# Kernel optimization log

Measured on AMD Instinct MI355X. Metric: run time of the kernel, lower is better.

The kernel has to match this reference:

```python
import jax, jax.numpy as jnp
import numpy as np

# dims
N_USER = 30000; N_ITEM = 30000; HID = 256; HEADS = 4; DH = HID // HEADS
L = 2; E_BUYS = 200000
IMG_D = 512; TASTE_D = 768; NUTR_D = 20; LR = 64; IMG_RANK = 64
EPS = 1e-5
# node type order: 0=user 1=item 2=taste 3=intention 4=image
# edge type order: taste->item, intention->item, image->item, user->item (buys), item->user (bought_by)


def _bn(x, g, b):
    # nn.BatchNorm1d in training mode (biased variance), deterministic
    mu = jnp.mean(x, axis=0)
    var = jnp.mean((x - mu) ** 2, axis=0)
    return (x - mu) * jax.lax.rsqrt(var + EPS) * g + b


def _segment_softmax(logits, seg, n):
    m = jax.ops.segment_max(logits, seg, num_segments=n)
    m = jnp.where(jnp.isfinite(m), m, 0.0)
    e = jnp.exp(logits - m[seg])
    s = jax.ops.segment_sum(e, seg, num_segments=n)
    return e / (s[seg] + 1e-16)


def _model(p, user_id, item_id, buys_src, buys_dst):
    # --- encoders (dropout = identity in eval) ---
    xu = jax.nn.relu(_bn(p['user_emb'][user_id] @ p['user_W'] + p['user_b'], p['user_bn_g'], p['user_bn_b']))
    xi = jax.nn.relu(_bn(p['item_emb'][item_id] @ p['item_W'] + p['item_b'], p['item_bn_g'], p['item_bn_b']))
    ximg = (p['image_feat'] @ p['img_U']) @ p['img_V'] + p['img_b']  # LowRankLinear
    xt = p['taste_feat'] @ p['taste_W'] + p['taste_b']
    xn = p['intent_feat'] @ p['intent_W'] + p['intent_b']
    xs = [xu, xi, xt, xn, ximg]
    assoc = jnp.arange(N_ITEM, dtype=jnp.int32)
    # (src_type, dst_type, src_idx, dst_idx)
    edges = [(2, 1, assoc, assoc), (3, 1, assoc, assoc), (4, 1, assoc, assoc),
             (0, 1, buys_src, buys_dst), (1, 0, buys_dst, buys_src)]
    scale = 1.0 / np.sqrt(DH)
    n_of = [N_USER, N_ITEM]
    for l in range(L):
        k, q, v = [], [], []
        for t in range(5):
            kqv = xs[t] @ p['kqv_W'][l, t] + p['kqv_b'][l, t]
            kk, qq, vv = jnp.split(kqv, 3, axis=1)
            k.append(kk.reshape(-1, HEADS, DH))
            q.append(qq.reshape(-1, HEADS, DH))
            v.append(vv.reshape(-1, HEADS, DH))
        buf = {0: [], 1: []}
        for e, (s, d, si, di) in enumerate(edges):
            # relation-specific per-head transforms of source k/v (all src nodes, then gather)
            ke = jnp.einsum('nhd,hde->nhe', k[s], p['k_rel'][l, e])
            ve = jnp.einsum('nhd,hde->nhe', v[s], p['v_rel'][l, e])
            logit = jnp.sum(q[d][di] * ke[si], axis=-1) * p['p_rel'][l, e] * scale  # [E,H]
            buf[d].append((logit, ve[si], di))
        new_xs = list(xs)
        for d in (0, 1):  # dst node types: user, item
            logits = jnp.concatenate([b[0] for b in buf[d]], axis=0)
            msgs = jnp.concatenate([b[1] for b in buf[d]], axis=0)
            dsts = jnp.concatenate([b[2] for b in buf[d]], axis=0)
            alpha = _segment_softmax(logits, dsts, n_of[d])  # softmax over ALL incoming edges per dst node
            agg = jax.ops.segment_sum(alpha[:, :, None] * msgs, dsts, num_segments=n_of[d])
            o = jax.nn.gelu(agg.reshape(-1, HID), approximate=False) @ p['out_W'][l, d] + p['out_b'][l, d]
            sg = jax.nn.sigmoid(p['skip'][l, d])
            o = sg * o + (1.0 - sg) * xs[d]  # HGTConv learned skip
            o = o + xs[d]                    # MultiModalFusionGAT residual
            o = jax.nn.relu(_bn(o, p['fbn_g'][l, d], p['fbn_b'][l, d]))  # per-type BN+ReLU (dropout eval)
            new_xs[d] = o
        xs = new_xs  # taste/intention/image pass through unchanged
    return jnp.stack(xs, axis=0)  # [5, 30000, HID]


def setup_inputs():
    key = jax.random.key(0)
    ks = iter(jax.random.split(key, 48))
    def nrm(shape, scale=0.05):
        return jax.random.normal(next(ks), shape, dtype=jnp.float32) * scale
    z = lambda *s: jnp.zeros(s, jnp.float32)
    o = lambda *s: jnp.ones(s, jnp.float32)
    inp = {}
    inp['user_id'] = jnp.arange(N_USER, dtype=jnp.int32)
    inp['item_id'] = jnp.arange(N_ITEM, dtype=jnp.int32)
    inp['buys_src'] = jax.random.randint(next(ks), (E_BUYS,), 0, N_USER, dtype=jnp.int32)
    inp['buys_dst'] = jax.random.randint(next(ks), (E_BUYS,), 0, N_ITEM, dtype=jnp.int32)
    inp['image_feat'] = nrm((N_ITEM, IMG_D), 1.0)
    inp['taste_feat'] = nrm((N_ITEM, TASTE_D), 1.0)
    inp['intent_feat'] = nrm((N_ITEM, NUTR_D), 1.0)
    inp['user_emb'] = nrm((N_USER, LR), 0.1)
    inp['user_W'] = nrm((LR, HID)); inp['user_b'] = z(HID)
    inp['user_bn_g'] = o(HID); inp['user_bn_b'] = z(HID)
    inp['item_emb'] = nrm((N_ITEM, LR), 0.1)
    inp['item_W'] = nrm((LR, HID)); inp['item_b'] = z(HID)
    inp['item_bn_g'] = o(HID); inp['item_bn_b'] = z(HID)
    inp['img_U'] = nrm((IMG_D, IMG_RANK)); inp['img_V'] = nrm((IMG_RANK, HID)); inp['img_b'] = z(HID)
    inp['taste_W'] = nrm((TASTE_D, HID)); inp['taste_b'] = z(HID)
    inp['intent_W'] = nrm((NUTR_D, HID)); inp['intent_b'] = z(HID)
    inp['kqv_W'] = nrm((L, 5, HID, 3 * HID)); inp['kqv_b'] = z(L, 5, 3 * HID)
    inp['out_W'] = nrm((L, 5, HID, HID)); inp['out_b'] = z(L, 5, HID)
    inp['k_rel'] = nrm((L, 5, HEADS, DH, DH))
    inp['v_rel'] = nrm((L, 5, HEADS, DH, DH))
    inp['p_rel'] = o(L, 5, HEADS)
    inp['skip'] = o(L, 5)
    inp['fbn_g'] = o(L, 2, HID); inp['fbn_b'] = z(L, 2, HID)
    return inp


def reference(user_id, item_id, buys_src, buys_dst, image_feat, taste_feat, intent_feat,
              user_emb, user_W, user_b, user_bn_g, user_bn_b,
              item_emb, item_W, item_b, item_bn_g, item_bn_b,
              img_U, img_V, img_b, taste_W, taste_b, intent_W, intent_b,
              kqv_W, kqv_b, out_W, out_b, k_rel, v_rel, p_rel, skip, fbn_g, fbn_b):
    p = dict(image_feat=image_feat, taste_feat=taste_feat, intent_feat=intent_feat,
             user_emb=user_emb, user_W=user_W, user_b=user_b, user_bn_g=user_bn_g, user_bn_b=user_bn_b,
             item_emb=item_emb, item_W=item_W, item_b=item_b, item_bn_g=item_bn_g, item_bn_b=item_bn_b,
             img_U=img_U, img_V=img_V, img_b=img_b, taste_W=taste_W, taste_b=taste_b,
             intent_W=intent_W, intent_b=intent_b, kqv_W=kqv_W, kqv_b=kqv_b, out_W=out_W, out_b=out_b,
             k_rel=k_rel, v_rel=v_rel, p_rel=p_rel, skip=skip, fbn_g=fbn_g, fbn_b=fbn_b)
    return _model(p, user_id, item_id, buys_src, buys_dst)
```

## Files before the change

### kernel.cpp

```cpp
#include <hip/hip_runtime.h>
#include <math.h>

#define HID 256
#define EBUY 200000
#define NNODE 30000
#define MP 30080
static const size_t S  = (size_t)NNODE * HID;
static const size_t SP = (size_t)MP * HID;

typedef __attribute__((ext_vector_type(8))) short  short8;
typedef __attribute__((ext_vector_type(4))) float  f32x4;

#define OFF_TASTE 0
#define OFF_INT   196608
#define OFF_IMGU  204800
#define OFF_IMGV  237568
#define OFF_USER  253952
#define OFF_ITEM  270336
#define OFF_OUTW  286720
#define WENC_TOT  548864

__device__ __forceinline__ float gelu_f(float x) {
    return 0.5f * x * (1.0f + erff(x * 0.70710678118654752f));
}
__device__ __forceinline__ unsigned short f2bf(float f) {
    unsigned u = __float_as_uint(f);
    u = (u + 0x7FFFu + ((u >> 16) & 1u)) >> 16;
    return (unsigned short)u;
}
__device__ __forceinline__ float b2f(unsigned short us) {
    return __uint_as_float((unsigned)us << 16);
}
__device__ __forceinline__ void gl_lds16(const unsigned short* g, unsigned short* l) {
    __builtin_amdgcn_global_load_lds(
        (const __attribute__((address_space(1))) unsigned int*)g,
        (__attribute__((address_space(3))) unsigned int*)l, 16, 0, 0);
}

__global__ void conv_pad(const float* __restrict__ in, unsigned short* __restrict__ o,
                         int M, int K, int Kpad)
{
    int i = blockIdx.x * 256 + threadIdx.x;
    if (i >= M * Kpad) return;
    int r = i / Kpad, k = i % Kpad;
    o[i] = (k < K) ? f2bf(in[(size_t)r * K + k]) : (unsigned short)0;
}

__global__ void wtconv_all(const float* __restrict__ taste_W, const float* __restrict__ intent_W,
                           const float* __restrict__ img_U, const float* __restrict__ img_V,
                           const float* __restrict__ user_W, const float* __restrict__ item_W,
                           const float* __restrict__ out_W, unsigned short* __restrict__ WENC)
{
    int i = blockIdx.x * 256 + threadIdx.x;
    if (i >= WENC_TOT) return;
    const float* W; int K, N, Kpad, idx;
    if (i < OFF_INT)        { W = taste_W;  K = 768; N = 256; Kpad = 768; idx = i - OFF_TASTE; }
    else if (i < OFF_IMGU)  { W = intent_W; K = 20;  N = 256; Kpad = 32;  idx = i - OFF_INT; }
    else if (i < OFF_IMGV)  { W = img_U;    K = 512; N = 64;  Kpad = 512; idx = i - OFF_IMGU; }
    else if (i < OFF_USER)  { W = img_V;    K = 64;  N = 256; Kpad = 64;  idx = i - OFF_IMGV; }
    else if (i < OFF_ITEM)  { W = user_W;   K = 64;  N = 256; Kpad = 64;  idx = i - OFF_USER; }
    else if (i < OFF_OUTW)  { W = item_W;   K = 64;  N = 256; Kpad = 64;  idx = i - OFF_ITEM; }
    else {
        int k = (i - OFF_OUTW) >> 16;
        int l = k >> 1, d = k & 1;
        W = out_W + (size_t)(l * 5 + d) * 65536;
        K = 256; N = 256; Kpad = 256; idx = (i - OFF_OUTW) & 65535;
    }
    int n = idx / Kpad, kk = idx % Kpad;
    WENC[i] = (kk < K) ? f2bf(W[(size_t)kk * N + n]) : (unsigned short)0;
}

__global__ void build_kqv(const float* __restrict__ kqv_W, const float* __restrict__ kqv_b,
                          const float* __restrict__ k_rel, const float* __restrict__ v_rel,
                          unsigned short* __restrict__ WKV, float* __restrict__ bKV,
                          unsigned short* __restrict__ WQ, float* __restrict__ bQ)
{
    int s = blockIdx.y;
    int l = s / 5, t = s % 5;
    static const int es[5] = {3, 4, 0, 1, 2};
    int e = es[t];
    int tid = blockIdx.x * 256 + threadIdx.x;
    if (tid >= 257 * 768) return;
    int r = tid / 768, c = tid % 768;
    int cb = c >> 8, cc = c & 255;
    int h = cc >> 6, dd = cc & 63;
    const float* W = kqv_W + (size_t)s * 196608;
    const float* bv = kqv_b + (size_t)s * 768;
    const float* Wrow = (r < 256) ? (W + (size_t)r * 768) : bv;
    if (cb == 1) {
        if (t >= 2) return;
        float outv = Wrow[256 + cc];
        if (r < 256) WQ[(size_t)(l * 2 + t) * 65536 + (size_t)cc * 256 + r] = f2bf(outv);
        else         bQ[(l * 2 + t) * 256 + cc] = outv;
        return;
    }
    const float* R = ((cb == 0) ? k_rel : v_rel) + (size_t)(l * 5 + e) * 16384 + (size_t)h * 4096;
    int sb = (cb == 0) ? 0 : 512;
    float sum = 0.f;
    #pragma unroll 8
    for (int d = 0; d < 64; ++d)
        sum += Wrow[sb + h * 64 + d] * R[d * 64 + dd];
    int col = (cb == 0) ? cc : 256 + cc;
    if (r < 256) WKV[(size_t)s * 131072 + (size_t)col * 256 + r] = f2bf(sum);
    else         bKV[s * 512 + col] = sum;
}

template<int AF32, int GATH2, int BSEL, int EPI>
__launch_bounds__(256)
__global__ void gemm_mfma(const void* __restrict__ Ap, const void* __restrict__ Ap2,
                          const int* __restrict__ g1, const int* __restrict__ g2,
                          const unsigned short* __restrict__ BT0, int bStride,
                          const float* __restrict__ bias0, const float* __restrict__ bias1,
                          int biasStride,
                          float* __restrict__ D0, unsigned short* __restrict__ Db,
                          unsigned short* __restrict__ Db2,
                          int M, int N, int K,
                          const float* __restrict__ skipP, const float* __restrict__ resid,
                          float* __restrict__ bns)
{
    __shared__ union {
        unsigned short AB[4][4096];
        unsigned short O[16384];
    } sm;
    const int tid = threadIdx.x;
    const int gx = gridDim.x;
    int bid = blockIdx.y * gx + blockIdx.x;
    {
        int nwg = gx * gridDim.y;
        int q = nwg >> 3, r = nwg & 7;
        int xc = bid & 7, i = bid >> 3;
        int base = (xc < r) ? xc * (q + 1) : r * (q + 1) + (xc - r) * q;
        bid = base + i;
    }
    const int bx = bid % gx, by = bid / gx;
    const int row0 = by * 128, col0 = bx * 128;
    const int wid = tid >> 6, lane = tid & 63;
    const int wr = wid >> 1, wc = wid & 1;
    const int l16 = lane & 15, kg = lane >> 4;
    const int tt = (BSEL || GATH2) ? (by / 235) : 0;

    const unsigned short* BT = BT0 + (size_t)tt * bStride;
    const float* bias = bias0;
    if (GATH2)              bias = tt ? bias1 : bias0;
    else if (BSEL && bias0) bias = bias0 + (size_t)tt * biasStride;

    f32x4 acc[4][4];
    const f32x4 zero = {0.f, 0.f, 0.f, 0.f};
    #pragma unroll
    for (int i = 0; i < 4; ++i)
        #pragma unroll
        for (int j = 0; j < 4; ++j) acc[i][j] = zero;

    const int lrow = lane >> 2, lchk = lane & 3;
    int cB0 = min(col0 + wid * 32 + lrow, N - 1);
    int cB1 = min(col0 + wid * 32 + 16 + lrow, N - 1);
    const unsigned short* Bp0 = BT + (size_t)cB0 * K + lchk * 8;
    const unsigned short* Bp1 = BT + (size_t)cB1 * K + lchk * 8;
    const int ofs0 = wid * 1024;
    const int ofs1 = wid * 1024 + 512;

    const unsigned short* Ap0b = nullptr; const unsigned short* Ap1b = nullptr;
    const float* Af0 = nullptr; const float* Af1 = nullptr;
    const int rA0 = tid >> 2, rA1 = (tid >> 2) + 64;
    const int q0 = tid & 3;
    if (GATH2) {
        int lr0 = row0 + rA0 - tt * MP; if (lr0 >= NNODE) lr0 = NNODE - 1;
        int lr1 = row0 + rA1 - tt * MP; if (lr1 >= NNODE) lr1 = NNODE - 1;
        const int* gA = tt ? g2 : g1;
        const float* Abase = tt ? (const float*)Ap2 : (const float*)Ap;
        Af0 = Abase + (size_t)gA[lr0] * K;
        Af1 = Abase + (size_t)gA[lr1] * K;
    } else if (AF32) {
        Af0 = (const float*)Ap + (size_t)min(row0 + rA0, M - 1) * K;
        Af1 = (const float*)Ap + (size_t)min(row0 + rA1, M - 1) * K;
    } else {
        int rr0 = min(row0 + wid * 32 + lrow, M - 1);
        int rr1 = min(row0 + wid * 32 + 16 + lrow, M - 1);
        Ap0b = (const unsigned short*)Ap + (size_t)rr0 * K + lchk * 8;
        Ap1b = (const unsigned short*)Ap + (size_t)rr1 * K + lchk * 8;
    }

    const int nt = K >> 5;
    int cur = 0;
    #define STAGE(c, k0) do { \
        if (AF32 || GATH2) { \
            float4 x0 = *(const float4*)&Af0[(k0) + q0 * 8]; \
            float4 x1 = *(const float4*)&Af0[(k0) + q0 * 8 + 4]; \
            float4 y0 = *(const float4*)&Af1[(k0) + q0 * 8]; \
            float4 y1 = *(const float4*)&Af1[(k0) + q0 * 8 + 4]; \
            ushort4 u0 = {f2bf(x0.x), f2bf(x0.y), f2bf(x0.z), f2bf(x0.w)}; \
            ushort4 u1 = {f2bf(x1.x), f2bf(x1.y), f2bf(x1.z), f2bf(x1.w)}; \
            ushort4 w0 = {f2bf(y0.x), f2bf(y0.y), f2bf(y0.z), f2bf(y0.w)}; \
            ushort4 w1 = {f2bf(y1.x), f2bf(y1.y), f2bf(y1.z), f2bf(y1.w)}; \
            *(ushort4*)&sm.AB[c][rA0 * 32 + q0 * 8]     = u0; \
            *(ushort4*)&sm.AB[c][rA0 * 32 + q0 * 8 + 4] = u1; \
            *(ushort4*)&sm.AB[c][rA1 * 32 + q0 * 8]     = w0; \
            *(ushort4*)&sm.AB[c][rA1 * 32 + q0 * 8 + 4] = w1; \
        } else { \
            gl_lds16(Ap0b + (k0), &sm.AB[c][ofs0]); \
            gl_lds16(Ap1b + (k0), &sm.AB[c][ofs1]); \
        } \
        gl_lds16(Bp0 + (k0), &sm.AB[2 + (c)][ofs0]); \
        gl_lds16(Bp1 + (k0), &sm.AB[2 + (c)][ofs1]); \
    } while (0)

    STAGE(0, 0);
    __syncthreads();
    for (int s = 0; s < nt; ++s) {
        if (s + 1 < nt) STAGE(cur ^ 1, (s + 1) * 32);
        short8 af[4], bfr[4];
        #pragma unroll
        for (int i = 0; i < 4; ++i) {
            af[i]  = *(const short8*)&sm.AB[cur][(wr * 64 + i * 16 + l16) * 32 + kg * 8];
            bfr[i] = *(const short8*)&sm.AB[2 + cur][(wc * 64 + i * 16 + l16) * 32 + kg * 8];
        }
        #pragma unroll
        for (int i = 0; i < 4; ++i)
            #pragma unroll
            for (int j = 0; j < 4; ++j)
                acc[i][j] = __builtin_amdgcn_mfma_f32_16x16x32_bf16(af[i], bfr[j], acc[i][j], 0, 0, 0);
        __syncthreads();
        cur ^= 1;
    }
    #undef STAGE

    float sg = 0.f;
    if (EPI == 2) sg = 1.f / (1.f + __expf(-skipP[0]));
    #pragma unroll
    for (int j = 0; j < 4; ++j) {
        int lc = wc * 64 + j * 16 + l16;
        int cc = col0 + lc;
        float cs = 0.f, cs2 = 0.f;
        float bv = (bias && cc < N) ? bias[cc] : 0.f;
        #pragma unroll
        for (int i = 0; i < 4; ++i) {
            #pragma unroll
            for (int r = 0; r < 4; ++r) {
                int lr = wr * 64 + i * 16 + kg * 4 + r;
                int rr = row0 + lr;
                float v = acc[i][j][r] + bv;
                if (EPI == 0) {
                    if (D0 && cc < N && rr < M) D0[(size_t)rr * N + cc] = v;
                    sm.O[lr * 128 + ((((lc >> 3) ^ (lr & 7)) << 3) | (lc & 7))] = f2bf(v);
                } else if (EPI == 4 || EPI == 5) {
                    sm.O[lr * 128 + ((((lc >> 3) ^ (lr & 7)) << 3) | (lc & 7))] = f2bf(v);
                } else if (EPI == 6) {
                    D0[(size_t)rr * 256 + cc] = v;
                } else if (EPI == 2) {
                    if (rr < M) {
                        float xo = resid[(size_t)rr * 256 + cc];
                        float o = sg * v + (2.f - sg) * xo;
                        D0[(size_t)rr * 256 + cc] = o;
                        cs += o; cs2 += o * o;
                    }
                }
            }
        }
        if (EPI == 2) {
            cs  += __shfl_xor(cs, 16);  cs  += __shfl_xor(cs, 32);
            cs2 += __shfl_xor(cs2, 16); cs2 += __shfl_xor(cs2, 32);
            if (kg == 0 && cc < N) {
                atomicAdd(&bns[cc], cs);
                atomicAdd(&bns[256 + cc], cs2);
            }
        }
    }
    if (EPI == 0 || EPI == 4 || EPI == 5) {
        __syncthreads();
        unsigned short* T; int ldN, cofs;
        if (EPI == 4)      { T = (col0 < 256) ? Db : Db2; ldN = 256; cofs = col0 & 255; }
        else if (EPI == 5) { T = Db; ldN = 256; cofs = col0; }
        else               { T = Db; ldN = N;   cofs = col0; }
        int nloc = N - col0; if (nloc > 128) nloc = 128;
        if (nloc >= 128) {
            int lr = tid >> 1, half = tid & 1;
            int rr = row0 + lr;
            if (EPI != 0 || rr < M) {
                uint4* dst = (uint4*)&T[(size_t)rr * ldN + cofs + half * 64];
                #pragma unroll
                for (int c = 0; c < 8; ++c) {
                    int ch = half * 8 + c;
                    dst[c] = *(const uint4*)&sm.O[lr * 128 + ((ch ^ (lr & 7)) << 3)];
                }
            }
        } else {
            if (tid < 128) {
                int lr = tid, rr = row0 + lr;
                if (rr < M) {
                    uint4* dst = (uint4*)&T[(size_t)rr * ldN + cofs];
                    #pragma unroll
                    for (int c = 0; c < 8; ++c)
                        dst[c] = *(const uint4*)&sm.O[lr * 128 + ((c ^ (lr & 7)) << 3)];
                }
            }
        }
    }
}

__global__ void edge_hist2(const int* __restrict__ dstk, const int* __restrict__ srck,
                           int* __restrict__ cnt)
{
    int j = blockIdx.x * 256 + threadIdx.x;
    if (j < EBUY) atomicAdd(&cnt[dstk[j]], 1);
    else if (j < 2 * EBUY) atomicAdd(&cnt[NNODE + srck[j - EBUY]], 1);
}

#define SCAN_NB 30
#define SCAN_CH 1000
__global__ void scan_part(const int* __restrict__ cnt, int* __restrict__ bt)
{
    int set = blockIdx.y;
    const int* c = cnt + set * NNODE;
    int b = blockIdx.x;
    int i = b * SCAN_CH + threadIdx.x;
    int v = (threadIdx.x < SCAN_CH && i < NNODE) ? c[i] : 0;
    __shared__ int wsum[16];
    int lane = threadIdx.x & 63, wv = threadIdx.x >> 6;
    for (int o = 32; o; o >>= 1) v += __shfl_down(v, o);
    if (lane == 0) wsum[wv] = v;
    __syncthreads();
    if (threadIdx.x == 0) {
        int s = 0;
        for (int w = 0; w < 16; ++w) s += wsum[w];
        bt[set * 32 + b] = s;
    }
}

__global__ void scan_mid(int* __restrict__ bt, int* __restrict__ off_i, int* __restrict__ off_u)
{
    int set = threadIdx.x;
    if (set >= 2) return;
    int* b = bt + set * 32;
    int s = 0;
    for (int i = 0; i < SCAN_NB; ++i) { int c = b[i]; b[i] = s; s += c; }
    (set ? off_u : off_i)[NNODE] = s;
}

__global__ void scan_final(const int* __restrict__ cnt, const int* __restrict__ bt,
                           int* __restrict__ off_i, int* __restrict__ off_u,
                           int* __restrict__ cur_i, int* __restrict__ cur_u)
{
    int set = blockIdx.y;
    const int* c = cnt + set * NNODE;
    int* off = set ? off_u : off_i;
    int* cur = set ? cur_u : cur_i;
    int b = blockIdx.x;
    int i = b * SCAN_CH + threadIdx.x;
    int v = (threadIdx.x < SCAN_CH && i < NNODE) ? c[i] : 0;
    int lane = threadIdx.x & 63, wv = threadIdx.x >> 6;
    int x = v;
    for (int o = 1; o < 64; o <<= 1) { int t = __shfl_up(x, o); if (lane >= o) x += t; }
    __shared__ int wtot[16];
    if (lane == 63) wtot[wv] = x;
    __syncthreads();
    if (wv == 0) {
        int y = (lane < 16) ? wtot[lane] : 0;
        for (int o = 1; o < 16; o <<= 1) { int t = __shfl_up(y, o); if (lane >= o) y += t; }
        if (lane < 16) wtot[lane] = y;
    }
    __syncthreads();
    int wbase = (wv == 0) ? 0 : wtot[wv - 1];
    int excl = bt[set * 32 + b] + wbase + x - v;
    if (threadIdx.x < SCAN_CH && i < NNODE) { off[i] = excl; cur[i] = excl; }
}

__global__ void edge_place2(const int* __restrict__ dstk, const int* __restrict__ srck,
                            int* __restrict__ cur_i, int* __restrict__ cur_u,
                            int* __restrict__ src_i, int* __restrict__ src_u)
{
    int j = blockIdx.x * 256 + threadIdx.x;
    if (j < EBUY) {
        int pos = atomicAdd(&cur_i[dstk[j]], 1);
        src_i[pos] = srck[j];
    } else if (j < 2 * EBUY) {
        int j2 = j - EBUY;
        int pos = atomicAdd(&cur_u[srck[j2]], 1);
        src_u[pos] = dstk[j2];
    }
}

template<int HAS_ASSOC>
__launch_bounds__(256)
__global__ void attn_gather(const unsigned short* __restrict__ Qd,
                            const unsigned short* __restrict__ KEs,
                            const unsigned short* __restrict__ VEs,
                            const unsigned short* __restrict__ KEa,
                            const unsigned short* __restrict__ VEa,
                            const int* __restrict__ roff, const int* __restrict__ srcArr,
                            const float* __restrict__ pR,
                            unsigned short* __restrict__ AGGb)
{
    int wid = (blockIdx.x * 256 + threadIdx.x) >> 6;
    int lane = threadIdx.x & 63;
    if (wid >= NNODE) return;
    int h = lane >> 4;

    ushort4 qb = *(const ushort4*)(Qd + (size_t)wid * 256 + lane * 4);
    float4 q = {b2f(qb.x), b2f(qb.y), b2f(qb.z), b2f(qb.w)};
    float m = -INFINITY, s = 0.f;
    float4 acc = {0.f, 0.f, 0.f, 0.f};

    if (HAS_ASSOC) {
        #pragma unroll
        for (int e = 0; e < 3; ++e) {
            ushort4 kb = *(const ushort4*)(KEa + (size_t)e * SP + (size_t)wid * 256 + lane * 4);
            float d = q.x * b2f(kb.x) + q.y * b2f(kb.y) + q.z * b2f(kb.z) + q.w * b2f(kb.w);
            for (int off = 8; off; off >>= 1) d += __shfl_xor(d, off, 16);
            float lg = d * pR[e * 4 + h] * 0.125f;
            ushort4 vv = *(const ushort4*)(VEa + (size_t)e * SP + (size_t)wid * 256 + lane * 4);
            float mn = fmaxf(m, lg);
            float so = __expf(m - mn);
            float ev = __expf(lg - mn);
            s = s * so + ev;
            acc.x = acc.x * so + ev * b2f(vv.x);
            acc.y = acc.y * so + ev * b2f(vv.y);
            acc.z = acc.z * so + ev * b2f(vv.z);
            acc.w = acc.w * so + ev * b2f(vv.w);
            m = mn;
        }
    }

    float pb = pR[(HAS_ASSOC ? 12 : 16) + h] * 0.125f;
    int j1 = roff[wid + 1];
    for (int j = roff[wid]; j < j1; ++j) {
        int src = srcArr[j];
        ushort4 kb = *(const ushort4*)(KEs + (size_t)src * 256 + lane * 4);
        float d = q.x * b2f(kb.x) + q.y * b2f(kb.y) + q.z * b2f(kb.z) + q.w * b2f(kb.w);
        for (int off = 8; off; off >>= 1) d += __shfl_xor(d, off, 16);
        float lg = d * pb;
        ushort4 vv = *(const ushort4*)(VEs + (size_t)src * 256 + lane * 4);
        float mn = fmaxf(m, lg);
        float so = __expf(m - mn);
        float ev = __expf(lg - mn);
        s = s * so + ev;
        acc.x = acc.x * so + ev * b2f(vv.x);
        acc.y = acc.y * so + ev * b2f(vv.y);
        acc.z = acc.z * so + ev * b2f(vv.z);
        acc.w = acc.w * so + ev * b2f(vv.w);
        m = mn;
    }

    float inv = 1.f / (s + 1e-16f);
    ushort4 o4;
    o4.x = f2bf(gelu_f(acc.x * inv));
    o4.y = f2bf(gelu_f(acc.y * inv));
    o4.z = f2bf(gelu_f(acc.z * inv));
    o4.w = f2bf(gelu_f(acc.w * inv));
    *(ushort4*)(AGGb + (size_t)wid * 256 + lane * 4) = o4;
}

#define BNB 512
__global__ void bn_stats2(const float* __restrict__ SCRf, float* __restrict__ part)
{
    int tt = blockIdx.y;
    const float* x = SCRf + (size_t)tt * SP;
    int col = threadIdx.x;
    int b = blockIdx.x;
    float s = 0.f, s2 = 0.f;
    int r = b;
    for (; r + 3 * BNB < NNODE; r += 4 * BNB) {
        float v0 = x[(size_t)r * 256 + col];
        float v1 = x[(size_t)(r + BNB) * 256 + col];
        float v2 = x[(size_t)(r + 2 * BNB) * 256 + col];
        float v3 = x[(size_t)(r + 3 * BNB) * 256 + col];
        s += v0 + v1 + v2 + v3;
        s2 += v0 * v0 + v1 * v1 + v2 * v2 + v3 * v3;
    }
    for (; r < NNODE; r += BNB) {
        float v = x[(size_t)r * 256 + col];
        s += v; s2 += v * v;
    }
    part[((size_t)tt * BNB + b) * 512 + col] = s;
    part[((size_t)tt * BNB + b) * 512 + 256 + col] = s2;
}

__global__ void bn_fin2(const float* __restrict__ part,
                        const float* __restrict__ g0, const float* __restrict__ b0,
                        const float* __restrict__ g1, const float* __restrict__ b1,
                        float* __restrict__ scsh)
{
    int tid = threadIdx.x;
    int tt = tid >> 8, col = tid & 255;
    const float* p = part + (size_t)tt * BNB * 512;
    float s = 0.f, s2 = 0.f;
    #pragma unroll 4
    for (int b = 0; b < BNB; ++b) { s += p[b * 512 + col]; s2 += p[b * 512 + 256 + col]; }
    float mu = s / (float)NNODE;
    float var = s2 / (float)NNODE - mu * mu;
    float sc = rsqrtf(var + 1e-5f) * (tt ? g1 : g0)[col];
    scsh[tt * 512 + col] = sc;
    scsh[tt * 512 + 256 + col] = (tt ? b1 : b0)[col] - mu * sc;
}

__global__ void bn_apply2(const float* __restrict__ SCRf, const float* __restrict__ scsh,
                          float* __restrict__ out, unsigned short* __restrict__ XBall)
{
    const int Q4 = NNODE * 64;
    for (int i = blockIdx.x * 256 + threadIdx.x; i < 2 * Q4; i += gridDim.x * 256) {
        int tt = (i >= Q4) ? 1 : 0;
        int local = i - tt * Q4;
        int c4 = local & 63;
        float4 sc4 = *(const float4*)&scsh[tt * 512 + c4 * 4];
        float4 sh4 = *(const float4*)&scsh[tt * 512 + 256 + c4 * 4];
        float4 v = ((const float4*)(SCRf + (size_t)tt * SP))[local];
        v.x = fmaxf(v.x * sc4.x + sh4.x, 0.f);
        v.y = fmaxf(v.y * sc4.y + sh4.y, 0.f);
        v.z = fmaxf(v.z * sc4.z + sh4.z, 0.f);
        v.w = fmaxf(v.w * sc4.w + sh4.w, 0.f);
        ((float4*)(out + (size_t)tt * S))[local] = v;
        ushort4 u = {f2bf(v.x), f2bf(v.y), f2bf(v.z), f2bf(v.w)};
        ((ushort4*)(XBall + (size_t)tt * SP))[local] = u;
    }
}

__global__ void bn_find(const float* __restrict__ bns, const float* __restrict__ g,
                        const float* __restrict__ b_, float* __restrict__ scsh)
{
    int col = threadIdx.x;
    float s = bns[col], s2 = bns[256 + col];
    float mu = s / (float)NNODE;
    float var = s2 / (float)NNODE - mu * mu;
    float sc = rsqrtf(var + 1e-5f) * g[col];
    scsh[col] = sc;
    scsh[256 + col] = b_[col] - mu * sc;
}

__global__ void bn_apply1(const float* __restrict__ x, const float* __restrict__ scsh,
                          float* __restrict__ y, unsigned short* __restrict__ yb)
{
    const int Q4 = NNODE * 64;
    int c4 = threadIdx.x & 63;
    float4 sc4 = *(const float4*)&scsh[c4 * 4];
    float4 sh4 = *(const float4*)&scsh[256 + c4 * 4];
    for (int i = blockIdx.x * 256 + threadIdx.x; i < Q4; i += gridDim.x * 256) {
        float4 v = ((const float4*)x)[i];
        v.x = fmaxf(v.x * sc4.x + sh4.x, 0.f);
        v.y = fmaxf(v.y * sc4.y + sh4.y, 0.f);
        v.z = fmaxf(v.z * sc4.z + sh4.z, 0.f);
        v.w = fmaxf(v.w * sc4.w + sh4.w, 0.f);
        ((float4*)y)[i] = v;
        ushort4 u = {f2bf(v.x), f2bf(v.y), f2bf(v.z), f2bf(v.w)};
        ((ushort4*)yb)[i] = u;
    }
}

extern "C" void kernel_launch(void* const* d_in, const int* in_sizes, int n_in,
                              void* d_out, int out_size, void* d_ws, size_t ws_size,
                              hipStream_t stream)
{
    const int*   user_id    = (const int*)d_in[0];
    const int*   item_id    = (const int*)d_in[1];
    const int*   buys_src   = (const int*)d_in[2];
    const int*   buys_dst   = (const int*)d_in[3];
    const float* image_feat = (const float*)d_in[4];
    const float* taste_feat = (const float*)d_in[5];
    const float* intent_feat= (const float*)d_in[6];
    const float* user_emb   = (const float*)d_in[7];
    const float* user_W     = (const float*)d_in[8];
    const float* user_b     = (const float*)d_in[9];
    const float* user_bn_g  = (const float*)d_in[10];
    const float* user_bn_b  = (const float*)d_in[11];
    const float* item_emb   = (const float*)d_in[12];
    const float* item_W     = (const float*)d_in[13];
    const float* item_b     = (const float*)d_in[14];
    const float* item_bn_g  = (const float*)d_in[15];
    const float* item_bn_b  = (const float*)d_in[16];
    const float* img_U      = (const float*)d_in[17];
    const float* img_V      = (const float*)d_in[18];
    const float* img_b      = (const float*)d_in[19];
    const float* taste_W    = (const float*)d_in[20];
    const float* taste_b    = (const float*)d_in[21];
    const float* intent_W   = (const float*)d_in[22];
    const float* intent_b   = (const float*)d_in[23];
    const float* kqv_W      = (const float*)d_in[24];
    const float* kqv_b      = (const float*)d_in[25];
    const float* out_W      = (const float*)d_in[26];
    const float* out_b      = (const float*)d_in[27];
    const float* k_rel      = (const float*)d_in[28];
    const float* v_rel      = (const float*)d_in[29];
    const float* p_rel      = (const float*)d_in[30];
    const float* skip       = (const float*)d_in[31];
    const float* fbn_g      = (const float*)d_in[32];
    const float* fbn_b      = (const float*)d_in[33];

    float* out = (float*)d_out;
    float* ws  = (float*)d_ws;

    float* SCRf = ws;
    float* BNSp = SCRf + 2 * SP;
    float* BNS  = BNSp + 2 * BNB * 512;
    float* SCSH = BNS + 512;
    float* bKV  = SCSH + 1024;
    float* bQ   = bKV + 5120;
    unsigned short* QB    = (unsigned short*)(bQ + 1024);
    unsigned short* XBall = QB + 2 * SP;
    unsigned short* KEall = XBall + 5 * SP;
    unsigned short* VEall = KEall + 5 * SP;
    unsigned short* AGB   = VEall + 5 * SP;
    unsigned short* IMB   = AGB + S;
    unsigned short* IPB   = IMB + (size_t)NNODE * 64;
    unsigned short* WKV   = IPB + (size_t)NNODE * 32;
    unsigned short* WQ    = WKV + 1310720;
    unsigned short* WENC  = WQ + 262144;
    int* cnt   = (int*)(WENC + WENC_TOT);
    int* off_i = cnt + 2 * NNODE;
    int* off_u = off_i + NNODE + 1;
    int* cur_i = off_u + NNODE + 1;
    int* cur_u = cur_i + NNODE;
    int* src_i = cur_u + NNODE;
    int* src_u = src_i + EBUY;
    int* bt    = src_u + EBUY;

    size_t need = (size_t)((char*)(bt + 64) - (char*)ws);
    if (ws_size < need) return;

    hipMemsetAsync(cnt, 0, 2 * NNODE * 4, stream);
    edge_hist2<<<(2 * EBUY + 255) / 256, 256, 0, stream>>>(buys_dst, buys_src, cnt);
    scan_part<<<dim3(SCAN_NB, 2), 1024, 0, stream>>>(cnt, bt);
    scan_mid<<<1, 64, 0, stream>>>(bt, off_i, off_u);
    scan_final<<<dim3(SCAN_NB, 2), 1024, 0, stream>>>(cnt, bt, off_i, off_u, cur_i, cur_u);
    edge_place2<<<(2 * EBUY + 255) / 256, 256, 0, stream>>>(buys_dst, buys_src, cur_i, cur_u, src_i, src_u);

    wtconv_all<<<(WENC_TOT + 255) / 256, 256, 0, stream>>>(taste_W, intent_W, img_U, img_V,
                                                           user_W, item_W, out_W, WENC);
    build_kqv<<<dim3(771, 10), 256, 0, stream>>>(kqv_W, kqv_b, k_rel, v_rel, WKV, bKV, WQ, bQ);
    conv_pad<<<(NNODE * 32 + 255) / 256, 256, 0, stream>>>(intent_feat, IPB, NNODE, 20, 32);

    hipLaunchKernelGGL((gemm_mfma<1,0,0,0>), dim3(2,235), dim3(256), 0, stream,
        taste_feat, nullptr, nullptr, nullptr, WENC + OFF_TASTE, 0, taste_b, nullptr, 0,
        out + 2*S, XBall + 2*SP, nullptr, NNODE, 256, 768, nullptr, nullptr, nullptr);
    hipLaunchKernelGGL((gemm_mfma<0,0,0,0>), dim3(2,235), dim3(256), 0, stream,
        IPB, nullptr, nullptr, nullptr, WENC + OFF_INT, 0, intent_b, nullptr, 0,
        out + 3*S, XBall + 3*SP, nullptr, NNODE, 256, 32, nullptr, nullptr, nullptr);
    hipLaunchKernelGGL((gemm_mfma<1,0,0,0>), dim3(1,235), dim3(256), 0, stream,
        image_feat, nullptr, nullptr, nullptr, WENC + OFF_IMGU, 0, nullptr, nullptr, 0,
        nullptr, IMB, nullptr, NNODE, 64, 512, nullptr, nullptr, nullptr);
    hipLaunchKernelGGL((gemm_mfma<0,0,0,0>), dim3(2,235), dim3(256), 0, stream,
        IMB, nullptr, nullptr, nullptr, WENC + OFF_IMGV, 0, img_b, nullptr, 0,
        out + 4*S, XBall + 4*SP, nullptr, NNODE, 256, 64, nullptr, nullptr, nullptr);
    hipLaunchKernelGGL((gemm_mfma<1,1,1,6>), dim3(2,470), dim3(256), 0, stream,
        user_emb, item_emb, user_id, item_id, WENC + OFF_USER, 16384, user_b, item_b, 0,
        SCRf, nullptr, nullptr, 2*MP, 256, 64, nullptr, nullptr, nullptr);
    bn_stats2<<<dim3(BNB, 2), 256, 0, stream>>>(SCRf, BNSp);
    bn_fin2<<<1, 512, 0, stream>>>(BNSp, user_bn_g, user_bn_b, item_bn_g, item_bn_b, SCSH);
    bn_apply2<<<960, 256, 0, stream>>>(SCRf, SCSH, out, XBall);

    for (int l = 0; l < 2; ++l) {
        hipLaunchKernelGGL((gemm_mfma<0,0,1,4>), dim3(4, 5*235), dim3(256), 0, stream,
            XBall, nullptr, nullptr, nullptr, WKV + (size_t)l*5*131072, 131072,
            bKV + l*5*512, nullptr, 512, nullptr, KEall, VEall,
            5*MP, 512, 256, nullptr, nullptr, nullptr);
        hipLaunchKernelGGL((gemm_mfma<0,0,1,5>), dim3(2, 2*235), dim3(256), 0, stream,
            XBall, nullptr, nullptr, nullptr, WQ + (size_t)l*2*65536, 65536,
            bQ + l*2*256, nullptr, 256, nullptr, QB, nullptr,
            2*MP, 256, 256, nullptr, nullptr, nullptr);
        hipLaunchKernelGGL((attn_gather<1>), dim3((NNODE*64 + 255)/256), dim3(256), 0, stream,
            QB + SP, KEall, VEall, KEall + 2*SP, VEall + 2*SP, off_i, src_i,
            p_rel + l*20, AGB);
        hipMemsetAsync(BNS, 0, 512 * 4, stream);
        hipLaunchKernelGGL((gemm_mfma<0,0,0,2>), dim3(2,235), dim3(256), 0, stream,
            AGB, nullptr, nullptr, nullptr, WENC + OFF_OUTW + (size_t)(l*2+1)*65536, 0,
            out_b + (l*5+1)*256, nullptr, 0, SCRf, nullptr, nullptr,
            NNODE, 256, 256, skip + (l*5+1), out + S, BNS);
        bn_find<<<1, 256, 0, stream>>>(BNS, fbn_g + (l*2+1)*256, fbn_b + (l*2+1)*256, SCSH);
        bn_apply1<<<960, 256, 0, stream>>>(SCRf, SCSH, out + S, XBall + SP);
        hipLaunchKernelGGL((attn_gather<0>), dim3((NNODE*64 + 255)/256), dim3(256), 0, stream,
            QB, KEall + SP, VEall + SP, nullptr, nullptr, off_u, src_u,
            p_rel + l*20, AGB);
        hipMemsetAsync(BNS, 0, 512 * 4, stream);
        hipLaunchKernelGGL((gemm_mfma<0,0,0,2>), dim3(2,235), dim3(256), 0, stream,
            AGB, nullptr, nullptr, nullptr, WENC + OFF_OUTW + (size_t)(l*2+0)*65536, 0,
            out_b + (l*5+0)*256, nullptr, 0, SCRf, nullptr, nullptr,
            NNODE, 256, 256, skip + (l*5+0), out, BNS);
        bn_find<<<1, 256, 0, stream>>>(BNS, fbn_g + (l*2+0)*256, fbn_b + (l*2+0)*256, SCSH);
        bn_apply1<<<960, 256, 0, stream>>>(SCRf, SCSH, out, XBall);
    }
}
```

Measured before the change: 1.085 ms.

## Pipeline bf16 GEMM with explicit vmcnt waits and prefetch edge gathers

Splits the GEMM main loop into an fp32-convert path and a bf16 direct-to-LDS path. The bf16 path replaces __syncthreads with explicit s_waitcnt vmcnt plus raw s_barrier, so the next tile's global-to-LDS loads stay in flight while the current tile is computed, and it raises wave priority around the MFMA block. In the attention aggregation, the next edge's K/V rows are loaded one iteration ahead to hide gather latency. The hand-written waitcnt values depend on exactly four outstanding loads per stage, which is fragile if the compiler inserts other memory operations.

```diff
diff --git a/kernel.cpp b/kernel.cpp
--- a/kernel.cpp
+++ b/kernel.cpp
@@ -182,47 +182,83 @@
 
     const int nt = K >> 5;
     int cur = 0;
-    #define STAGE(c, k0) do { \
-        if (AF32 || GATH2) { \
-            float4 x0 = *(const float4*)&Af0[(k0) + q0 * 8]; \
-            float4 x1 = *(const float4*)&Af0[(k0) + q0 * 8 + 4]; \
-            float4 y0 = *(const float4*)&Af1[(k0) + q0 * 8]; \
-            float4 y1 = *(const float4*)&Af1[(k0) + q0 * 8 + 4]; \
-            ushort4 u0 = {f2bf(x0.x), f2bf(x0.y), f2bf(x0.z), f2bf(x0.w)}; \
-            ushort4 u1 = {f2bf(x1.x), f2bf(x1.y), f2bf(x1.z), f2bf(x1.w)}; \
-            ushort4 w0 = {f2bf(y0.x), f2bf(y0.y), f2bf(y0.z), f2bf(y0.w)}; \
-            ushort4 w1 = {f2bf(y1.x), f2bf(y1.y), f2bf(y1.z), f2bf(y1.w)}; \
-            *(ushort4*)&sm.AB[c][rA0 * 32 + q0 * 8]     = u0; \
-            *(ushort4*)&sm.AB[c][rA0 * 32 + q0 * 8 + 4] = u1; \
-            *(ushort4*)&sm.AB[c][rA1 * 32 + q0 * 8]     = w0; \
-            *(ushort4*)&sm.AB[c][rA1 * 32 + q0 * 8 + 4] = w1; \
-        } else { \
-            gl_lds16(Ap0b + (k0), &sm.AB[c][ofs0]); \
-            gl_lds16(Ap1b + (k0), &sm.AB[c][ofs1]); \
-        } \
+
+    #define STAGE_F32(c, k0) do { \
+        float4 x0 = *(const float4*)&Af0[(k0) + q0 * 8]; \
+        float4 x1 = *(const float4*)&Af0[(k0) + q0 * 8 + 4]; \
+        float4 y0 = *(const float4*)&Af1[(k0) + q0 * 8]; \
+        float4 y1 = *(const float4*)&Af1[(k0) + q0 * 8 + 4]; \
+        ushort4 u0 = {f2bf(x0.x), f2bf(x0.y), f2bf(x0.z), f2bf(x0.w)}; \
+        ushort4 u1 = {f2bf(x1.x), f2bf(x1.y), f2bf(x1.z), f2bf(x1.w)}; \
+        ushort4 w0 = {f2bf(y0.x), f2bf(y0.y), f2bf(y0.z), f2bf(y0.w)}; \
+        ushort4 w1 = {f2bf(y1.x), f2bf(y1.y), f2bf(y1.z), f2bf(y1.w)}; \
+        *(ushort4*)&sm.AB[c][rA0 * 32 + q0 * 8]     = u0; \
+        *(ushort4*)&sm.AB[c][rA0 * 32 + q0 * 8 + 4] = u1; \
+        *(ushort4*)&sm.AB[c][rA1 * 32 + q0 * 8]     = w0; \
+        *(ushort4*)&sm.AB[c][rA1 * 32 + q0 * 8 + 4] = w1; \
         gl_lds16(Bp0 + (k0), &sm.AB[2 + (c)][ofs0]); \
         gl_lds16(Bp1 + (k0), &sm.AB[2 + (c)][ofs1]); \
     } while (0)
 
-    STAGE(0, 0);
-    __syncthreads();
-    for (int s = 0; s < nt; ++s) {
-        if (s + 1 < nt) STAGE(cur ^ 1, (s + 1) * 32);
-        short8 af[4], bfr[4];
-        #pragma unroll
-        for (int i = 0; i < 4; ++i) {
-            af[i]  = *(const short8*)&sm.AB[cur][(wr * 64 + i * 16 + l16) * 32 + kg * 8];
-            bfr[i] = *(const short8*)&sm.AB[2 + cur][(wc * 64 + i * 16 + l16) * 32 + kg * 8];
+    #define STAGE_A(c, k0) do { \
+        gl_lds16(Ap0b + (k0), &sm.AB[c][ofs0]); \
+        gl_lds16(Ap1b + (k0), &sm.AB[c][ofs1]); \
+        gl_lds16(Bp0 + (k0), &sm.AB[2 + (c)][ofs0]); \
+        gl_lds16(Bp1 + (k0), &sm.AB[2 + (c)][ofs1]); \
+    } while (0)
+
+    #define LOADFRAG(c) do { \
+        _Pragma("unroll") \
+        for (int i = 0; i < 4; ++i) { \
+            af[i]  = *(const short8*)&sm.AB[c][(wr * 64 + i * 16 + l16) * 32 + kg * 8]; \
+            bfr[i] = *(const short8*)&sm.AB[2 + (c)][(wc * 64 + i * 16 + l16) * 32 + kg * 8]; \
+        } \
+    } while (0)
+
+    #define MMAS() do { \
+        _Pragma("unroll") \
+        for (int i = 0; i < 4; ++i) \
+            _Pragma("unroll") \
+            for (int j = 0; j < 4; ++j) \
+                acc[i][j] = __builtin_amdgcn_mfma_f32_16x16x32_bf16(af[i], bfr[j], acc[i][j], 0, 0, 0); \
+    } while (0)
+
+    if (AF32 || GATH2) {
+        STAGE_F32(0, 0);
+        __syncthreads();
+        for (int s = 0; s < nt; ++s) {
+            if (s + 1 < nt) STAGE_F32(cur ^ 1, (s + 1) * 32);
+            short8 af[4], bfr[4];
+            LOADFRAG(cur);
+            MMAS();
+            __syncthreads();
+            cur ^= 1;
         }
-        #pragma unroll
-        for (int i = 0; i < 4; ++i)
-            #pragma unroll
-            for (int j = 0; j < 4; ++j)
-                acc[i][j] = __builtin_amdgcn_mfma_f32_16x16x32_bf16(af[i], bfr[j], acc[i][j], 0, 0, 0);
-        __syncthreads();
-        cur ^= 1;
-    }
-    #undef STAGE
+    } else {
+        STAGE_A(0, 0);
+        for (int s = 0; s < nt; ++s) {
+            if (s + 1 < nt) {
+                STAGE_A(cur ^ 1, (s + 1) * 32);
+                asm volatile("s_waitcnt vmcnt(4)" ::: "memory");
+            } else {
+                asm volatile("s_waitcnt vmcnt(0)" ::: "memory");
+            }
+            __builtin_amdgcn_s_barrier();
+            asm volatile("" ::: "memory");
+            short8 af[4], bfr[4];
+            LOADFRAG(cur);
+            __builtin_amdgcn_s_setprio(1);
+            MMAS();
+            __builtin_amdgcn_s_setprio(0);
+            __builtin_amdgcn_s_barrier();
+            asm volatile("" ::: "memory");
+            cur ^= 1;
+        }
+    }
+    #undef STAGE_F32
+    #undef STAGE_A
+    #undef LOADFRAG
+    #undef MMAS
 
     float sg = 0.f;
     if (EPI == 2) sg = 1.f / (1.f + __expf(-skipP[0]));
@@ -421,22 +457,31 @@
     }
 
     float pb = pR[(HAS_ASSOC ? 12 : 16) + h] * 0.125f;
-    int j1 = roff[wid + 1];
-    for (int j = roff[wid]; j < j1; ++j) {
-        int src = srcArr[j];
-        ushort4 kb = *(const ushort4*)(KEs + (size_t)src * 256 + lane * 4);
-        float d = q.x * b2f(kb.x) + q.y * b2f(kb.y) + q.z * b2f(kb.z) + q.w * b2f(kb.w);
+    int j0 = roff[wid], j1 = roff[wid + 1];
+    ushort4 kb = {0,0,0,0}, vv = {0,0,0,0};
+    if (j0 < j1) {
+        int src0 = srcArr[j0];
+        kb = *(const ushort4*)(KEs + (size_t)src0 * 256 + lane * 4);
+        vv = *(const ushort4*)(VEs + (size_t)src0 * 256 + lane * 4);
+    }
+    for (int j = j0; j < j1; ++j) {
+        ushort4 ckb = kb, cvv = vv;
+        if (j + 1 < j1) {
+            int ns = srcArr[j + 1];
+            kb = *(const ushort4*)(KEs + (size_t)ns * 256 + lane * 4);
+            vv = *(const ushort4*)(VEs + (size_t)ns * 256 + lane * 4);
+        }
+        float d = q.x * b2f(ckb.x) + q.y * b2f(ckb.y) + q.z * b2f(ckb.z) + q.w * b2f(ckb.w);
         for (int off = 8; off; off >>= 1) d += __shfl_xor(d, off, 16);
         float lg = d * pb;
-        ushort4 vv = *(const ushort4*)(VEs + (size_t)src * 256 + lane * 4);
         float mn = fmaxf(m, lg);
         float so = __expf(m - mn);
         float ev = __expf(lg - mn);
         s = s * so + ev;
-        acc.x = acc.x * so + ev * b2f(vv.x);
-        acc.y = acc.y * so + ev * b2f(vv.y);
-        acc.z = acc.z * so + ev * b2f(vv.z);
-        acc.w = acc.w * so + ev * b2f(vv.w);
+        acc.x = acc.x * so + ev * b2f(cvv.x);
+        acc.y = acc.y * so + ev * b2f(cvv.y);
+        acc.z = acc.z * so + ev * b2f(cvv.z);
+        acc.w = acc.w * so + ev * b2f(cvv.w);
         m = mn;
     }
 
```

Measured after the change: 1.039 ms. -4.3%, faster.
